# Kernel optimization log

Measured on AMD Instinct MI355X. Metric: run time of the kernel, lower is better.

## Reference

```python
import jax, jax.numpy as jnp
import numpy as np

N = 100000
E = 1600000
D_IN = 128
D_H = 128
D_OUT = 64
BN_EPS = 1e-5


def setup_inputs() -> dict:
    key = jax.random.key(0)
    ks = jax.random.split(key, 32)
    inp = {}
    inp["x"] = jax.random.normal(ks[0], (N, D_IN), dtype=jnp.float32)
    inp["edge_index"] = jax.random.randint(ks[1], (2, E), 0, N, dtype=jnp.int32)
    def lin(k, fan_in, fan_out):
        b = 1.0 / np.sqrt(fan_in)
        return jax.random.uniform(k, (fan_in, fan_out), jnp.float32, -b, b)
    # conv0: MLP [128,128,128]
    inp["W1_0"] = lin(ks[2], D_IN, D_H); inp["b1_0"] = jnp.zeros((D_H,), jnp.float32)
    inp["W2_0"] = lin(ks[3], D_H, D_H);  inp["b2_0"] = jnp.zeros((D_H,), jnp.float32)
    # conv1: MLP [128,128,128]
    inp["W1_1"] = lin(ks[4], D_H, D_H);  inp["b1_1"] = jnp.zeros((D_H,), jnp.float32)
    inp["W2_1"] = lin(ks[5], D_H, D_H);  inp["b2_1"] = jnp.zeros((D_H,), jnp.float32)
    # conv2 (last): MLP [128,128,64]
    inp["W1_2"] = lin(ks[6], D_H, D_H);  inp["b1_2"] = jnp.zeros((D_H,), jnp.float32)
    inp["W2_2"] = lin(ks[7], D_H, D_OUT); inp["b2_2"] = jnp.zeros((D_OUT,), jnp.float32)
    # BatchNorm (eval-mode) params for the 2 hidden layers
    for i, kk in zip((0, 1), (ks[8], ks[9])):
        inp[f"g{i}"] = jnp.ones((D_H,), jnp.float32)
        inp[f"be{i}"] = jnp.zeros((D_H,), jnp.float32)
        inp[f"m{i}"] = jax.random.normal(kk, (D_H,), jnp.float32) * 0.1
        inp[f"v{i}"] = jnp.ones((D_H,), jnp.float32)
    return inp


def _gin_conv(x, src, dst, W1, b1, W2, b2):
    # sum aggregation over incoming edges: out_i = x_i + sum_{j->i} x_j  (eps=0)
    agg = x + jax.ops.segment_sum(x[src], dst, num_segments=N)
    h = jax.nn.relu(agg @ W1 + b1)  # MLP hidden (dropout inactive in eval)
    return h @ W2 + b2


def _bn(h, g, be, m, v):
    return (h - m) * jax.lax.rsqrt(v + BN_EPS) * g + be


def reference(x, edge_index, W1_0, b1_0, W2_0, b2_0, W1_1, b1_1, W2_1, b2_1,
              W1_2, b1_2, W2_2, b2_2, g0, be0, m0, v0, g1, be1, m1, v1):
    src, dst = edge_index[0], edge_index[1]
    # layer 0
    out = _gin_conv(x, src, dst, W1_0, b1_0, W2_0, b2_0)
    out = _bn(out, g0, be0, m0, v0)
    x = jax.nn.relu(out) + x  # downsample is identity (in==hidden)
    # layer 1
    out = _gin_conv(x, src, dst, W1_1, b1_1, W2_1, b2_1)
    out = _bn(out, g1, be1, m1, v1)
    x = jax.nn.relu(out) + x
    # last conv + log_softmax
    out = _gin_conv(x, src, dst, W1_2, b1_2, W2_2, b2_2)
    return jax.nn.log_softmax(out, axis=-1)
```

## Files before the change

kernel.cpp:

```cpp
#include <hip/hip_runtime.h>
#include <math.h>

#define NN 100000
#define NE 1600000
#define BN_EPS 1e-5f
#define NB 782
#define BCAP 4096
#define EPB 4096
#define NEB ((NE + EPB - 1) / EPB)
#define CVB 12500

typedef short bf16x8 __attribute__((ext_vector_type(8)));
typedef float f32x4 __attribute__((ext_vector_type(4)));
typedef float f32x2 __attribute__((ext_vector_type(2)));
typedef unsigned short ushort;
typedef ushort us8 __attribute__((ext_vector_type(8)));
typedef ushort us4 __attribute__((ext_vector_type(4)));
typedef unsigned ui2 __attribute__((ext_vector_type(2)));

__device__ __forceinline__ ushort f2bf(float f) {
    unsigned u = __float_as_uint(f);
    unsigned r = (u + 0x7FFFu + ((u >> 16) & 1u)) >> 16;
    return (ushort)r;
}
__device__ __forceinline__ float bf2f(ushort h) { return __uint_as_float(((unsigned)h) << 16); }

__device__ __forceinline__ void fp8x8_f32(ui2 q, float* f) {
    f32x2 p;
    p = __builtin_amdgcn_cvt_pk_f32_fp8((int)q[0], false); f[0] = p[0]; f[1] = p[1];
    p = __builtin_amdgcn_cvt_pk_f32_fp8((int)q[0], true);  f[2] = p[0]; f[3] = p[1];
    p = __builtin_amdgcn_cvt_pk_f32_fp8((int)q[1], false); f[4] = p[0]; f[5] = p[1];
    p = __builtin_amdgcn_cvt_pk_f32_fp8((int)q[1], true);  f[6] = p[0]; f[7] = p[1];
}
__device__ __forceinline__ ui2 f32_fp8x8(const float* f) {
    int d0 = __builtin_amdgcn_cvt_pk_fp8_f32(f[0], f[1], 0, false);
    d0 = __builtin_amdgcn_cvt_pk_fp8_f32(f[2], f[3], d0, true);
    int d1 = __builtin_amdgcn_cvt_pk_fp8_f32(f[4], f[5], 0, false);
    d1 = __builtin_amdgcn_cvt_pk_fp8_f32(f[6], f[7], d1, true);
    ui2 r; r[0] = (unsigned)d0; r[1] = (unsigned)d1; return r;
}

__global__ __launch_bounds__(256) void prep1_k(const int* __restrict__ ei, int* __restrict__ bcur,
                                               unsigned* __restrict__ packed,
                                               const float* __restrict__ x, ushort* __restrict__ xb,
                                               unsigned* __restrict__ xq) {
    __shared__ int h[NB];
    if (blockIdx.x >= NEB) {
        int i = (blockIdx.x - NEB) * 256 + threadIdx.x;
        float4 v = ((const float4*)x)[i];
        us4 o;
        o[0] = f2bf(v.x); o[1] = f2bf(v.y); o[2] = f2bf(v.z); o[3] = f2bf(v.w);
        ((us4*)xb)[i] = o;
        int d = __builtin_amdgcn_cvt_pk_fp8_f32(v.x, v.y, 0, false);
        d = __builtin_amdgcn_cvt_pk_fp8_f32(v.z, v.w, d, true);
        xq[i] = (unsigned)d;
        return;
    }
    for (int i = threadIdx.x; i < NB; i += 256) h[i] = 0;
    __syncthreads();
    int base = blockIdx.x * EPB;
    for (int i = threadIdx.x; i < EPB; i += 256) {
        int e = base + i;
        if (e < NE) atomicAdd(&h[ei[NE + e] >> 7], 1);
    }
    __syncthreads();
    for (int i = threadIdx.x; i < NB; i += 256) {
        int c = h[i];
        if (c) h[i] = (i << 12) + atomicAdd(&bcur[i], c);
    }
    __syncthreads();
    for (int i = threadIdx.x; i < EPB; i += 256) {
        int e = base + i;
        if (e < NE) {
            int d = ei[NE + e];
            int b = d >> 7;
            int pos = atomicAdd(&h[b], 1);
            packed[pos] = (unsigned)ei[e] | ((unsigned)(d & 127) << 17);
        }
    }
}

__global__ __launch_bounds__(256) void prep2_k(
    unsigned* __restrict__ packed, const int* __restrict__ bcur,
    int* __restrict__ rpS, int* __restrict__ rpE, int* __restrict__ perm,
    const float* __restrict__ Wa, const float* __restrict__ Wb, const float* __restrict__ Wc,
    const float* __restrict__ Wd, const float* __restrict__ We, const float* __restrict__ Wf_,
    ushort* __restrict__ Fa, ushort* __restrict__ Fb, ushort* __restrict__ Fc,
    ushort* __restrict__ Fd, ushort* __restrict__ Fe, ushort* __restrict__ Ff) {
    __shared__ unsigned ent[BCAP];
    __shared__ int hc[128], hb[128], sc[128];
    if (blockIdx.x >= NB) {
        int bb = blockIdx.x - NB;
        int which = bb >> 3, sub = bb & 7;
        const float* W; ushort* F; int DOUT = 128;
        switch (which) {
            case 0: W = Wa; F = Fa; break;
            case 1: W = Wb; F = Fb; break;
            case 2: W = Wc; F = Fc; break;
            case 3: W = Wd; F = Fd; break;
            case 4: W = We; F = Fe; break;
            default: W = Wf_; F = Ff; DOUT = 64; break;
        }
        int NT = DOUT / 16;
        int idx = sub * 256 + threadIdx.x;
        if (idx >= 4 * NT * 64) return;
        int l = idx & 63;
        int nt = (idx >> 6) % NT;
        int kt = idx / (NT * 64);
        int colw = nt * 16 + (l & 15);
        int k0 = kt * 32 + (l >> 4) * 8;
        us8 o;
#pragma unroll
        for (int e = 0; e < 8; ++e) o[e] = f2bf(W[(k0 + e) * DOUT + colw]);
        ((us8*)F)[idx] = o;
        return;
    }
    int t = threadIdx.x, b = blockIdx.x;
    int base = b << 12;
    int nb = bcur[b];
    if (nb > BCAP) nb = BCAP;
    for (int i = t; i < nb; i += 256) ent[i] = packed[base + i];
    if (t < 128) hc[t] = 0;
    __syncthreads();
    for (int i = t; i < nb; i += 256) atomicAdd(&hc[ent[i] >> 17], 1);
    __syncthreads();
    if (t < 128) sc[t] = hc[t];
    __syncthreads();
    for (int off = 1; off < 128; off <<= 1) {
        int u = 0;
        if (t < 128 && t >= off) u = sc[t - off];
        __syncthreads();
        if (t < 128) sc[t] += u;
        __syncthreads();
    }
    if (t < 128) {
        int ex = sc[t] - hc[t];
        hb[t] = ex;
        int node = b * 128 + t;
        if (node < NN) {
            rpS[node] = base + ex;
            rpE[node] = base + sc[t];
        }
    }
    __syncthreads();
    for (int i = t; i < nb; i += 256) {
        unsigned u = ent[i];
        int pos = atomicAdd(&hb[u >> 17], 1);
        packed[base + pos] = u & 0x1FFFFu;
    }
    if (t < 128) {
        int half = t >> 6, li = t & 63;
        int mydeg = (b * 128 + t < NN) ? hc[t] : -1;
        int rank = 0;
#pragma unroll 8
        for (int j = 0; j < 64; ++j) {
            int oj = half * 64 + j;
            int od = (b * 128 + oj < NN) ? hc[oj] : -1;
            rank += (od > mydeg) || (od == mydeg && j < li);
        }
        perm[(b * 2 + half) * 64 + rank] = li;
    }
}

template <int FINAL>
__global__ __launch_bounds__(256, 4) void fused_k(
    const ushort* __restrict__ X, const unsigned* __restrict__ XQ,
    const int* __restrict__ rpS, const int* __restrict__ rpE,
    const unsigned* __restrict__ col, const int* __restrict__ perm,
    const ushort* __restrict__ W1f, const ushort* __restrict__ W2f,
    const float* __restrict__ b1, const float* __restrict__ b2,
    const float* __restrict__ bng, const float* __restrict__ bnb,
    const float* __restrict__ bnm, const float* __restrict__ bnv,
    ushort* __restrict__ outb, unsigned* __restrict__ outq, float* __restrict__ outf) {
    __shared__ ushort Alds[8192];
    __shared__ ushort Hlds[8192];
    __shared__ int pLds[64];
    const int t = threadIdx.x;
    const int w = t >> 6, l = t & 63;
    const int lrow = l & 15, lchk = l >> 4;
    const int R0 = blockIdx.x * 64;
    const us8* __restrict__ xv = (const us8*)X;
    const ui2* __restrict__ xq2 = (const ui2*)XQ;

    if (t < 64) pLds[t] = perm[blockIdx.x * 64 + t];
    __syncthreads();

    const int ch = t & 15;
#pragma unroll
    for (int it = 0; it < 4; ++it) {
        int nl = pLds[it * 16 + (t >> 4)];
        int node = R0 + nl;
        float a[8];
#pragma unroll
        for (int i = 0; i < 8; ++i) a[i] = 0.f;
        if (node < NN) {
            us8 self = xv[(size_t)node * 16 + ch];
#pragma unroll
            for (int i = 0; i < 8; ++i) a[i] = bf2f(self[i]);
            int p = rpS[node];
            const int pe = rpE[node];
            for (; p + 7 < pe; p += 8) {
                unsigned s[8];
#pragma unroll
                for (int u = 0; u < 8; ++u) s[u] = col[p + u];
                ui2 v[8];
#pragma unroll
                for (int u = 0; u < 8; ++u) v[u] = xq2[(size_t)s[u] * 16 + ch];
#pragma unroll
                for (int u = 0; u < 8; ++u) {
                    float f[8];
                    fp8x8_f32(v[u], f);
#pragma unroll
                    for (int i = 0; i < 8; ++i) a[i] += f[i];
                }
            }
            for (; p + 3 < pe; p += 4) {
                ui2 v0 = xq2[(size_t)col[p] * 16 + ch];
                ui2 v1 = xq2[(size_t)col[p + 1] * 16 + ch];
                ui2 v2 = xq2[(size_t)col[p + 2] * 16 + ch];
                ui2 v3 = xq2[(size_t)col[p + 3] * 16 + ch];
                float f0[8], f1[8], f2[8], f3[8];
                fp8x8_f32(v0, f0); fp8x8_f32(v1, f1); fp8x8_f32(v2, f2); fp8x8_f32(v3, f3);
#pragma unroll
                for (int i = 0; i < 8; ++i) a[i] += (f0[i] + f1[i]) + (f2[i] + f3[i]);
            }
            for (; p < pe; ++p) {
                ui2 v = xq2[(size_t)col[p] * 16 + ch];
                float f[8];
                fp8x8_f32(v, f);
#pragma unroll
                for (int i = 0; i < 8; ++i) a[i] += f[i];
            }
        }
        us8 o;
#pragma unroll
        for (int i = 0; i < 8; ++i) o[i] = f2bf(a[i]);
        int byte = (nl * 256 + ch * 16) ^ ((nl & 7) << 4);
        *(us8*)((char*)Alds + byte) = o;
    }

    const bf16x8* __restrict__ w1p = (const bf16x8*)W1f;
    bf16x8 w1r[2][4];
#pragma unroll
    for (int ntl = 0; ntl < 2; ++ntl)
#pragma unroll
        for (int kt = 0; kt < 4; ++kt)
            w1r[ntl][kt] = w1p[(kt * 8 + (2 * w + ntl)) * 64 + l];

    __syncthreads();

#pragma unroll
    for (int mt = 0; mt < 4; ++mt) {
        bf16x8 af[4];
#pragma unroll
        for (int kt = 0; kt < 4; ++kt) {
            int row = mt * 16 + lrow;
            int byte = (row * 256 + kt * 64 + lchk * 16) ^ ((row & 7) << 4);
            af[kt] = *(const bf16x8*)((char*)Alds + byte);
        }
        f32x4 acc[2] = {f32x4{0.f, 0.f, 0.f, 0.f}, f32x4{0.f, 0.f, 0.f, 0.f}};
#pragma unroll
        for (int kt = 0; kt < 4; ++kt)
#pragma unroll
            for (int ntl = 0; ntl < 2; ++ntl)
                acc[ntl] = __builtin_amdgcn_mfma_f32_16x16x32_bf16(af[kt], w1r[ntl][kt], acc[ntl], 0, 0, 0);
#pragma unroll
        for (int ntl = 0; ntl < 2; ++ntl) {
            int colb = (2 * w + ntl) * 16 + lrow;
            float bias = b1[colb];
#pragma unroll
            for (int r = 0; r < 4; ++r) {
                int rloc = mt * 16 + lchk * 4 + r;
                float hv = fmaxf(acc[ntl][r] + bias, 0.f);
                int byte = (rloc * 256 + colb * 2) ^ ((rloc & 7) << 4);
                *(ushort*)((char*)Hlds + byte) = f2bf(hv);
            }
        }
    }
    __syncthreads();

    if constexpr (FINAL == 0) {
        const bf16x8* __restrict__ w2p = (const bf16x8*)W2f;
        bf16x8 w2r[2][4];
#pragma unroll
        for (int ntl = 0; ntl < 2; ++ntl)
#pragma unroll
            for (int kt = 0; kt < 4; ++kt)
                w2r[ntl][kt] = w2p[(kt * 8 + (2 * w + ntl)) * 64 + l];
        float sc[2], of[2];
#pragma unroll
        for (int ntl = 0; ntl < 2; ++ntl) {
            int colb = (2 * w + ntl) * 16 + lrow;
            sc[ntl] = bng[colb] * rsqrtf(bnv[colb] + BN_EPS);
            of[ntl] = (b2[colb] - bnm[colb]) * sc[ntl] + bnb[colb];
        }
#pragma unroll
        for (int mt = 0; mt < 4; ++mt) {
            bf16x8 hf[4];
#pragma unroll
            for (int kt = 0; kt < 4; ++kt) {
                int row = mt * 16 + lrow;
                int byte = (row * 256 + kt * 64 + lchk * 16) ^ ((row & 7) << 4);
                hf[kt] = *(const bf16x8*)((char*)Hlds + byte);
            }
            f32x4 acc2[2] = {f32x4{0.f, 0.f, 0.f, 0.f}, f32x4{0.f, 0.f, 0.f, 0.f}};
#pragma unroll
            for (int kt = 0; kt < 4; ++kt)
#pragma unroll
                for (int ntl = 0; ntl < 2; ++ntl)
                    acc2[ntl] = __builtin_amdgcn_mfma_f32_16x16x32_bf16(hf[kt], w2r[ntl][kt], acc2[ntl], 0, 0, 0);
#pragma unroll
            for (int ntl = 0; ntl < 2; ++ntl) {
                int colb = (2 * w + ntl) * 16 + lrow;
#pragma unroll
                for (int r = 0; r < 4; ++r) {
                    int rloc = mt * 16 + lchk * 4 + r;
                    float o = fmaxf(acc2[ntl][r] * sc[ntl] + of[ntl], 0.f);
                    int byte = (rloc * 256 + colb * 2) ^ ((rloc & 7) << 4);
                    *(ushort*)((char*)Alds + byte) = f2bf(o);
                }
            }
        }
        __syncthreads();
        us8* __restrict__ ob8 = (us8*)outb;
        ui2* __restrict__ oq2 = (ui2*)outq;
#pragma unroll
        for (int j = 0; j < 4; ++j) {
            int i = t + 256 * j;
            int row = i >> 4, chunk = i & 15;
            int grow = R0 + row;
            if (grow < NN) {
                int byte = (row * 256 + chunk * 16) ^ ((row & 7) << 4);
                us8 h8 = *(const us8*)((char*)Alds + byte);
                us8 r8 = xv[(size_t)grow * 16 + chunk];
                float oo[8];
#pragma unroll
                for (int e = 0; e < 8; ++e) oo[e] = bf2f(h8[e]) + bf2f(r8[e]);
                us8 o8;
#pragma unroll
                for (int e = 0; e < 8; ++e) o8[e] = f2bf(oo[e]);
                ob8[(size_t)grow * 16 + chunk] = o8;
                oq2[(size_t)grow * 16 + chunk] = f32_fp8x8(oo);
            }
        }
    } else {
        const bf16x8* __restrict__ w2p = (const bf16x8*)W2f;
        bf16x8 hf[4];
#pragma unroll
        for (int kt = 0; kt < 4; ++kt) {
            int row = w * 16 + lrow;
            int byte = (row * 256 + kt * 64 + lchk * 16) ^ ((row & 7) << 4);
            hf[kt] = *(const bf16x8*)((char*)Hlds + byte);
        }
        f32x4 acc2[4];
#pragma unroll
        for (int nt = 0; nt < 4; ++nt) acc2[nt] = f32x4{0.f, 0.f, 0.f, 0.f};
#pragma unroll
        for (int kt = 0; kt < 4; ++kt)
#pragma unroll
            for (int nt = 0; nt < 4; ++nt)
                acc2[nt] = __builtin_amdgcn_mfma_f32_16x16x32_bf16(hf[kt], w2p[(kt * 4 + nt) * 64 + l], acc2[nt], 0, 0, 0);
        float bb[4];
#pragma unroll
        for (int nt = 0; nt < 4; ++nt) bb[nt] = b2[nt * 16 + lrow];
#pragma unroll
        for (int r = 0; r < 4; ++r) {
            float v0 = acc2[0][r] + bb[0], v1 = acc2[1][r] + bb[1];
            float v2 = acc2[2][r] + bb[2], v3 = acc2[3][r] + bb[3];
            float mx = fmaxf(fmaxf(v0, v1), fmaxf(v2, v3));
            for (int d = 1; d < 16; d <<= 1) mx = fmaxf(mx, __shfl_xor(mx, d));
            float sm = expf(v0 - mx) + expf(v1 - mx) + expf(v2 - mx) + expf(v3 - mx);
            for (int d = 1; d < 16; d <<= 1) sm += __shfl_xor(sm, d);
            float L = mx + logf(sm);
            int grow = R0 + w * 16 + lchk * 4 + r;
            if (grow < NN) {
                outf[(size_t)grow * 64 + 0 + lrow] = v0 - L;
                outf[(size_t)grow * 64 + 16 + lrow] = v1 - L;
                outf[(size_t)grow * 64 + 32 + lrow] = v2 - L;
                outf[(size_t)grow * 64 + 48 + lrow] = v3 - L;
            }
        }
    }
}

extern "C" void kernel_launch(void* const* d_in, const int* in_sizes, int n_in,
                              void* d_out, int out_size, void* d_ws, size_t ws_size,
                              hipStream_t stream) {
    const float* x = (const float*)d_in[0];
    const int* ei = (const int*)d_in[1];
    const float* W1_0 = (const float*)d_in[2];
    const float* b1_0 = (const float*)d_in[3];
    const float* W2_0 = (const float*)d_in[4];
    const float* b2_0 = (const float*)d_in[5];
    const float* W1_1 = (const float*)d_in[6];
    const float* b1_1 = (const float*)d_in[7];
    const float* W2_1 = (const float*)d_in[8];
    const float* b2_1 = (const float*)d_in[9];
    const float* W1_2 = (const float*)d_in[10];
    const float* b1_2 = (const float*)d_in[11];
    const float* W2_2 = (const float*)d_in[12];
    const float* b2_2 = (const float*)d_in[13];
    const float* g0 = (const float*)d_in[14];
    const float* be0 = (const float*)d_in[15];
    const float* m0 = (const float*)d_in[16];
    const float* v0 = (const float*)d_in[17];
    const float* g1 = (const float*)d_in[18];
    const float* be1 = (const float*)d_in[19];
    const float* m1 = (const float*)d_in[20];
    const float* v1 = (const float*)d_in[21];
    float* out = (float*)d_out;

    char* ws = (char*)d_ws;
    ushort* xb0 = (ushort*)(ws);
    ushort* xb1 = (ushort*)(ws + 25600000);
    unsigned* xq0 = (unsigned*)(ws + 51200000);
    unsigned* xq1 = (unsigned*)(ws + 64000000);
    unsigned* packed = (unsigned*)(ws + 76800000);
    int* rpS = (int*)(ws + 76800000 + 12812288);
    int* rpE = (int*)(ws + 76800000 + 12812288 + 400128);
    int* bcur = (int*)(ws + 76800000 + 12812288 + 800256);
    int* perm = (int*)(ws + 76800000 + 12812288 + 800256 + 4096);
    ushort* W10f = (ushort*)(ws + 76800000 + 12812288 + 800256 + 4096 + 401408);
    ushort* W20f = W10f + 16384;
    ushort* W11f = W20f + 16384;
    ushort* W21f = W11f + 16384;
    ushort* W12f = W21f + 16384;
    ushort* W22f = W12f + 16384;

    hipMemsetAsync(bcur, 0, NB * sizeof(int), stream);
    prep1_k<<<NEB + CVB, 256, 0, stream>>>(ei, bcur, packed, x, xb0, xq0);
    prep2_k<<<NB + 48, 256, 0, stream>>>(packed, bcur, rpS, rpE, perm,
                                         W1_0, W2_0, W1_1, W2_1, W1_2, W2_2,
                                         W10f, W20f, W11f, W21f, W12f, W22f);

    const int GG = (NN + 63) / 64;

    fused_k<0><<<GG, 256, 0, stream>>>(xb0, xq0, rpS, rpE, packed, perm, W10f, W20f, b1_0, b2_0,
                                       g0, be0, m0, v0, xb1, xq1, nullptr);
    fused_k<0><<<GG, 256, 0, stream>>>(xb1, xq1, rpS, rpE, packed, perm, W11f, W21f, b1_1, b2_1,
                                       g1, be1, m1, v1, xb0, xq0, nullptr);
    fused_k<1><<<GG, 256, 0, stream>>>(xb0, xq0, rpS, rpE, packed, perm, W12f, W22f, b1_2, b2_2,
                                       nullptr, nullptr, nullptr, nullptr, nullptr, nullptr, out);
}
```

Before: 227.3 us.

## Halve hidden LDS buffer by processing MLP in two row halves, raise occupancy

The fused GIN layer kernel now runs the two MLP matmuls in two passes of 32 rows each, so the hidden-activation LDS buffer shrinks from 8192 to 4096 bf16 elements. Launch bounds are raised from 4 to 6 blocks per CU to use the lower LDS footprint and hide gather latency. Weight repacking moves from prep2 to prep1 blocks to shorten prep2. The cost is an extra barrier per half, W2 fragments held in registers earlier, and possible register spills under the tighter occupancy bound.

```diff
diff --git a/kernel.cpp b/kernel.cpp
--- a/kernel.cpp
+++ b/kernel.cpp
@@ -43,8 +43,40 @@
 __global__ __launch_bounds__(256) void prep1_k(const int* __restrict__ ei, int* __restrict__ bcur,
                                                unsigned* __restrict__ packed,
                                                const float* __restrict__ x, ushort* __restrict__ xb,
-                                               unsigned* __restrict__ xq) {
+                                               unsigned* __restrict__ xq,
+                                               const float* __restrict__ Wa, const float* __restrict__ Wb,
+                                               const float* __restrict__ Wc, const float* __restrict__ Wd,
+                                               const float* __restrict__ We, const float* __restrict__ Wf_,
+                                               ushort* __restrict__ Fa, ushort* __restrict__ Fb,
+                                               ushort* __restrict__ Fc, ushort* __restrict__ Fd,
+                                               ushort* __restrict__ Fe, ushort* __restrict__ Ff) {
     __shared__ int h[NB];
+    if (blockIdx.x >= NEB + CVB) {
+        int bb = blockIdx.x - (NEB + CVB);
+        int which = bb >> 3, sub = bb & 7;
+        const float* W; ushort* F; int DOUT = 128;
+        switch (which) {
+            case 0: W = Wa; F = Fa; break;
+            case 1: W = Wb; F = Fb; break;
+            case 2: W = Wc; F = Fc; break;
+            case 3: W = Wd; F = Fd; break;
+            case 4: W = We; F = Fe; break;
+            default: W = Wf_; F = Ff; DOUT = 64; break;
+        }
+        int NT = DOUT / 16;
+        int idx = sub * 256 + threadIdx.x;
+        if (idx >= 4 * NT * 64) return;
+        int l = idx & 63;
+        int nt = (idx >> 6) % NT;
+        int kt = idx / (NT * 64);
+        int colw = nt * 16 + (l & 15);
+        int k0 = kt * 32 + (l >> 4) * 8;
+        us8 o;
+#pragma unroll
+        for (int e = 0; e < 8; ++e) o[e] = f2bf(W[(k0 + e) * DOUT + colw]);
+        ((us8*)F)[idx] = o;
+        return;
+    }
     if (blockIdx.x >= NEB) {
         int i = (blockIdx.x - NEB) * 256 + threadIdx.x;
         float4 v = ((const float4*)x)[i];
@@ -80,41 +112,11 @@
     }
 }
 
-__global__ __launch_bounds__(256) void prep2_k(
-    unsigned* __restrict__ packed, const int* __restrict__ bcur,
-    int* __restrict__ rpS, int* __restrict__ rpE, int* __restrict__ perm,
-    const float* __restrict__ Wa, const float* __restrict__ Wb, const float* __restrict__ Wc,
-    const float* __restrict__ Wd, const float* __restrict__ We, const float* __restrict__ Wf_,
-    ushort* __restrict__ Fa, ushort* __restrict__ Fb, ushort* __restrict__ Fc,
-    ushort* __restrict__ Fd, ushort* __restrict__ Fe, ushort* __restrict__ Ff) {
+__global__ __launch_bounds__(256) void prep2_k(unsigned* __restrict__ packed, const int* __restrict__ bcur,
+                                               int* __restrict__ rpS, int* __restrict__ rpE,
+                                               int* __restrict__ perm) {
     __shared__ unsigned ent[BCAP];
     __shared__ int hc[128], hb[128], sc[128];
-    if (blockIdx.x >= NB) {
-        int bb = blockIdx.x - NB;
-        int which = bb >> 3, sub = bb & 7;
-        const float* W; ushort* F; int DOUT = 128;
-        switch (which) {
-            case 0: W = Wa; F = Fa; break;
-            case 1: W = Wb; F = Fb; break;
-            case 2: W = Wc; F = Fc; break;
-            case 3: W = Wd; F = Fd; break;
-            case 4: W = We; F = Fe; break;
-            default: W = Wf_; F = Ff; DOUT = 64; break;
-        }
-        int NT = DOUT / 16;
-        int idx = sub * 256 + threadIdx.x;
-        if (idx >= 4 * NT * 64) return;
-        int l = idx & 63;
-        int nt = (idx >> 6) % NT;
-        int kt = idx / (NT * 64);
-        int colw = nt * 16 + (l & 15);
-        int k0 = kt * 32 + (l >> 4) * 8;
-        us8 o;
-#pragma unroll
-        for (int e = 0; e < 8; ++e) o[e] = f2bf(W[(k0 + e) * DOUT + colw]);
-        ((us8*)F)[idx] = o;
-        return;
-    }
     int t = threadIdx.x, b = blockIdx.x;
     int base = b << 12;
     int nb = bcur[b];
@@ -163,7 +165,7 @@
 }
 
 template <int FINAL>
-__global__ __launch_bounds__(256, 4) void fused_k(
+__global__ __launch_bounds__(256, 6) void fused_k(
     const ushort* __restrict__ X, const unsigned* __restrict__ XQ,
     const int* __restrict__ rpS, const int* __restrict__ rpE,
     const unsigned* __restrict__ col, const int* __restrict__ perm,
@@ -173,7 +175,7 @@
     const float* __restrict__ bnm, const float* __restrict__ bnv,
     ushort* __restrict__ outb, unsigned* __restrict__ outq, float* __restrict__ outf) {
     __shared__ ushort Alds[8192];
-    __shared__ ushort Hlds[8192];
+    __shared__ ushort Hlds[4096];
     __shared__ int pLds[64];
     const int t = threadIdx.x;
     const int w = t >> 6, l = t & 63;
@@ -246,82 +248,128 @@
 #pragma unroll
         for (int kt = 0; kt < 4; ++kt)
             w1r[ntl][kt] = w1p[(kt * 8 + (2 * w + ntl)) * 64 + l];
-
-    __syncthreads();
-
-#pragma unroll
-    for (int mt = 0; mt < 4; ++mt) {
-        bf16x8 af[4];
-#pragma unroll
-        for (int kt = 0; kt < 4; ++kt) {
-            int row = mt * 16 + lrow;
-            int byte = (row * 256 + kt * 64 + lchk * 16) ^ ((row & 7) << 4);
-            af[kt] = *(const bf16x8*)((char*)Alds + byte);
-        }
-        f32x4 acc[2] = {f32x4{0.f, 0.f, 0.f, 0.f}, f32x4{0.f, 0.f, 0.f, 0.f}};
-#pragma unroll
-        for (int kt = 0; kt < 4; ++kt)
-#pragma unroll
-            for (int ntl = 0; ntl < 2; ++ntl)
-                acc[ntl] = __builtin_amdgcn_mfma_f32_16x16x32_bf16(af[kt], w1r[ntl][kt], acc[ntl], 0, 0, 0);
-#pragma unroll
-        for (int ntl = 0; ntl < 2; ++ntl) {
-            int colb = (2 * w + ntl) * 16 + lrow;
-            float bias = b1[colb];
-#pragma unroll
-            for (int r = 0; r < 4; ++r) {
-                int rloc = mt * 16 + lchk * 4 + r;
-                float hv = fmaxf(acc[ntl][r] + bias, 0.f);
-                int byte = (rloc * 256 + colb * 2) ^ ((rloc & 7) << 4);
-                *(ushort*)((char*)Hlds + byte) = f2bf(hv);
-            }
-        }
-    }
-    __syncthreads();
-
+    bf16x8 w2r[2][4];
+    float sc[2], of[2];
     if constexpr (FINAL == 0) {
         const bf16x8* __restrict__ w2p = (const bf16x8*)W2f;
-        bf16x8 w2r[2][4];
 #pragma unroll
         for (int ntl = 0; ntl < 2; ++ntl)
 #pragma unroll
             for (int kt = 0; kt < 4; ++kt)
                 w2r[ntl][kt] = w2p[(kt * 8 + (2 * w + ntl)) * 64 + l];
-        float sc[2], of[2];
 #pragma unroll
         for (int ntl = 0; ntl < 2; ++ntl) {
             int colb = (2 * w + ntl) * 16 + lrow;
             sc[ntl] = bng[colb] * rsqrtf(bnv[colb] + BN_EPS);
             of[ntl] = (b2[colb] - bnm[colb]) * sc[ntl] + bnb[colb];
         }
-#pragma unroll
-        for (int mt = 0; mt < 4; ++mt) {
-            bf16x8 hf[4];
+    }
+
+    __syncthreads();
+
+#pragma unroll
+    for (int hh = 0; hh < 2; ++hh) {
+#pragma unroll
+        for (int mt = 0; mt < 2; ++mt) {
+            bf16x8 af[4];
 #pragma unroll
             for (int kt = 0; kt < 4; ++kt) {
-                int row = mt * 16 + lrow;
+                int row = hh * 32 + mt * 16 + lrow;
                 int byte = (row * 256 + kt * 64 + lchk * 16) ^ ((row & 7) << 4);
-                hf[kt] = *(const bf16x8*)((char*)Hlds + byte);
-            }
-            f32x4 acc2[2] = {f32x4{0.f, 0.f, 0.f, 0.f}, f32x4{0.f, 0.f, 0.f, 0.f}};
+                af[kt] = *(const bf16x8*)((char*)Alds + byte);
+            }
+            f32x4 acc[2] = {f32x4{0.f, 0.f, 0.f, 0.f}, f32x4{0.f, 0.f, 0.f, 0.f}};
 #pragma unroll
             for (int kt = 0; kt < 4; ++kt)
 #pragma unroll
                 for (int ntl = 0; ntl < 2; ++ntl)
-                    acc2[ntl] = __builtin_amdgcn_mfma_f32_16x16x32_bf16(hf[kt], w2r[ntl][kt], acc2[ntl], 0, 0, 0);
+                    acc[ntl] = __builtin_amdgcn_mfma_f32_16x16x32_bf16(af[kt], w1r[ntl][kt], acc[ntl], 0, 0, 0);
 #pragma unroll
             for (int ntl = 0; ntl < 2; ++ntl) {
                 int colb = (2 * w + ntl) * 16 + lrow;
+                float bias = b1[colb];
 #pragma unroll
                 for (int r = 0; r < 4; ++r) {
                     int rloc = mt * 16 + lchk * 4 + r;
-                    float o = fmaxf(acc2[ntl][r] * sc[ntl] + of[ntl], 0.f);
+                    float hv = fmaxf(acc[ntl][r] + bias, 0.f);
                     int byte = (rloc * 256 + colb * 2) ^ ((rloc & 7) << 4);
-                    *(ushort*)((char*)Alds + byte) = f2bf(o);
+                    *(ushort*)((char*)Hlds + byte) = f2bf(hv);
                 }
             }
         }
         __syncthreads();
+        if constexpr (FINAL == 0) {
+#pragma unroll
+            for (int mt = 0; mt < 2; ++mt) {
+                bf16x8 hf[4];
+#pragma unroll
+                for (int kt = 0; kt < 4; ++kt) {
+                    int rloc = mt * 16 + lrow;
+                    int byte = (rloc * 256 + kt * 64 + lchk * 16) ^ ((rloc & 7) << 4);
+                    hf[kt] = *(const bf16x8*)((char*)Hlds + byte);
+                }
+                f32x4 acc2[2] = {f32x4{0.f, 0.f, 0.f, 0.f}, f32x4{0.f, 0.f, 0.f, 0.f}};
+#pragma unroll
+                for (int kt = 0; kt < 4; ++kt)
+#pragma unroll
+                    for (int ntl = 0; ntl < 2; ++ntl)
+                        acc2[ntl] = __builtin_amdgcn_mfma_f32_16x16x32_bf16(hf[kt], w2r[ntl][kt], acc2[ntl], 0, 0, 0);
+#pragma unroll
+                for (int ntl = 0; ntl < 2; ++ntl) {
+                    int colb = (2 * w + ntl) * 16 + lrow;
+#pragma unroll
+                    for (int r = 0; r < 4; ++r) {
+                        int row = hh * 32 + mt * 16 + lchk * 4 + r;
+                        float o = fmaxf(acc2[ntl][r] * sc[ntl] + of[ntl], 0.f);
+                        int byte = (row * 256 + colb * 2) ^ ((row & 7) << 4);
+                        *(ushort*)((char*)Alds + byte) = f2bf(o);
+                    }
+                }
+            }
+        } else {
+            if (w < 2) {
+                const bf16x8* __restrict__ w2p = (const bf16x8*)W2f;
+                bf16x8 hf[4];
+#pragma unroll
+                for (int kt = 0; kt < 4; ++kt) {
+                    int rloc = w * 16 + lrow;
+                    int byte = (rloc * 256 + kt * 64 + lchk * 16) ^ ((rloc & 7) << 4);
+                    hf[kt] = *(const bf16x8*)((char*)Hlds + byte);
+                }
+                f32x4 acc2[4];
+#pragma unroll
+                for (int nt = 0; nt < 4; ++nt) acc2[nt] = f32x4{0.f, 0.f, 0.f, 0.f};
+#pragma unroll
+                for (int kt = 0; kt < 4; ++kt)
+#pragma unroll
+                    for (int nt = 0; nt < 4; ++nt)
+                        acc2[nt] = __builtin_amdgcn_mfma_f32_16x16x32_bf16(hf[kt], w2p[(kt * 4 + nt) * 64 + l], acc2[nt], 0, 0, 0);
+                float bb[4];
+#pragma unroll
+                for (int nt = 0; nt < 4; ++nt) bb[nt] = b2[nt * 16 + lrow];
+#pragma unroll
+                for (int r = 0; r < 4; ++r) {
+                    float v0 = acc2[0][r] + bb[0], v1 = acc2[1][r] + bb[1];
+                    float v2 = acc2[2][r] + bb[2], v3 = acc2[3][r] + bb[3];
+                    float mx = fmaxf(fmaxf(v0, v1), fmaxf(v2, v3));
+                    for (int d = 1; d < 16; d <<= 1) mx = fmaxf(mx, __shfl_xor(mx, d));
+                    float sm = expf(v0 - mx) + expf(v1 - mx) + expf(v2 - mx) + expf(v3 - mx);
+                    for (int d = 1; d < 16; d <<= 1) sm += __shfl_xor(sm, d);
+                    float L = mx + logf(sm);
+                    int grow = R0 + hh * 32 + w * 16 + lchk * 4 + r;
+                    if (grow < NN) {
+                        outf[(size_t)grow * 64 + 0 + lrow] = v0 - L;
+                        outf[(size_t)grow * 64 + 16 + lrow] = v1 - L;
+                        outf[(size_t)grow * 64 + 32 + lrow] = v2 - L;
+                        outf[(size_t)grow * 64 + 48 + lrow] = v3 - L;
+                    }
+                }
+            }
+        }
+        __syncthreads();
+    }
+
+    if constexpr (FINAL == 0) {
         us8* __restrict__ ob8 = (us8*)outb;
         ui2* __restrict__ oq2 = (ui2*)outq;
 #pragma unroll
@@ -341,43 +389,6 @@
                 for (int e = 0; e < 8; ++e) o8[e] = f2bf(oo[e]);
                 ob8[(size_t)grow * 16 + chunk] = o8;
                 oq2[(size_t)grow * 16 + chunk] = f32_fp8x8(oo);
-            }
-        }
-    } else {
-        const bf16x8* __restrict__ w2p = (const bf16x8*)W2f;
-        bf16x8 hf[4];
-#pragma unroll
-        for (int kt = 0; kt < 4; ++kt) {
-            int row = w * 16 + lrow;
-            int byte = (row * 256 + kt * 64 + lchk * 16) ^ ((row & 7) << 4);
-            hf[kt] = *(const bf16x8*)((char*)Hlds + byte);
-        }
-        f32x4 acc2[4];
-#pragma unroll
-        for (int nt = 0; nt < 4; ++nt) acc2[nt] = f32x4{0.f, 0.f, 0.f, 0.f};
-#pragma unroll
-        for (int kt = 0; kt < 4; ++kt)
-#pragma unroll
-            for (int nt = 0; nt < 4; ++nt)
-                acc2[nt] = __builtin_amdgcn_mfma_f32_16x16x32_bf16(hf[kt], w2p[(kt * 4 + nt) * 64 + l], acc2[nt], 0, 0, 0);
-        float bb[4];
-#pragma unroll
-        for (int nt = 0; nt < 4; ++nt) bb[nt] = b2[nt * 16 + lrow];
-#pragma unroll
-        for (int r = 0; r < 4; ++r) {
-            float v0 = acc2[0][r] + bb[0], v1 = acc2[1][r] + bb[1];
-            float v2 = acc2[2][r] + bb[2], v3 = acc2[3][r] + bb[3];
-            float mx = fmaxf(fmaxf(v0, v1), fmaxf(v2, v3));
-            for (int d = 1; d < 16; d <<= 1) mx = fmaxf(mx, __shfl_xor(mx, d));
-            float sm = expf(v0 - mx) + expf(v1 - mx) + expf(v2 - mx) + expf(v3 - mx);
-            for (int d = 1; d < 16; d <<= 1) sm += __shfl_xor(sm, d);
-            float L = mx + logf(sm);
-            int grow = R0 + w * 16 + lchk * 4 + r;
-            if (grow < NN) {
-                outf[(size_t)grow * 64 + 0 + lrow] = v0 - L;
-                outf[(size_t)grow * 64 + 16 + lrow] = v1 - L;
-                outf[(size_t)grow * 64 + 32 + lrow] = v2 - L;
-                outf[(size_t)grow * 64 + 48 + lrow] = v3 - L;
             }
         }
     }
@@ -428,10 +439,10 @@
     ushort* W22f = W12f + 16384;
 
     hipMemsetAsync(bcur, 0, NB * sizeof(int), stream);
-    prep1_k<<<NEB + CVB, 256, 0, stream>>>(ei, bcur, packed, x, xb0, xq0);
-    prep2_k<<<NB + 48, 256, 0, stream>>>(packed, bcur, rpS, rpE, perm,
-                                         W1_0, W2_0, W1_1, W2_1, W1_2, W2_2,
-                                         W10f, W20f, W11f, W21f, W12f, W22f);
+    prep1_k<<<NEB + CVB + 48, 256, 0, stream>>>(ei, bcur, packed, x, xb0, xq0,
+                                                W1_0, W2_0, W1_1, W2_1, W1_2, W2_2,
+                                                W10f, W20f, W11f, W21f, W12f, W22f);
+    prep2_k<<<NB, 256, 0, stream>>>(packed, bcur, rpS, rpE, perm);
 
     const int GG = (NN + 63) / 64;
 
```

New measurement: 365.2 us. 1.61x slower.
